# Performance work log

Measured on AMD Instinct MI355X. Metric: run time of the kernel, lower is better.

## Reference

```python
import jax, jax.numpy as jnp
import numpy as np

TEMPERATURE = 8.0  # sqrt(d_k=64)

def setup_inputs() -> dict:
    key = jax.random.key(0)
    kq, kk, kv = jax.random.split(key, 3)
    B, S, D = 32, 2048, 64
    q = jax.random.normal(kq, (B, S, D), dtype=jnp.float32)
    k = jax.random.normal(kk, (B, S, D), dtype=jnp.float32)
    v = jax.random.normal(kv, (B, S, D), dtype=jnp.float32)
    return {"q": q, "k": k, "v": v}

def reference(q, k, v):
    # scores: [B, S_q, S_k]
    attn = jnp.einsum('bqd,bkd->bqk', q, k) / TEMPERATURE
    attn = jax.nn.softmax(attn, axis=2)
    # dropout is identity in eval mode (deterministic reference baseline)
    output = jnp.einsum('bqk,bkd->bqd', attn, v)
    return (output, attn)
```

## Files before the change

kernel.cpp:

```cpp
#include <hip/hip_runtime.h>
#include <cstdint>
#include <cstddef>

#define B_    32
#define S_    2048
#define D_    64
#define QBLK  16
#define SLICE 264

typedef __attribute__((ext_vector_type(8))) short short8_t;
typedef __attribute__((ext_vector_type(4))) float f32x4;
typedef __attribute__((ext_vector_type(2))) unsigned u32x2;
typedef __attribute__((ext_vector_type(2))) float f32x2;

__device__ __forceinline__ short f2bf(float f) {
  union { float f; unsigned u; } x; x.f = f;
  unsigned u = x.u;
  u += 0x7fffu + ((u >> 16) & 1u);
  return (short)(u >> 16);
}
__device__ __forceinline__ float bf2f(unsigned s) {
  union { unsigned u; float f; } x;
  x.u = (s & 0xffffu) << 16;
  return x.f;
}

__global__ void convert_bf16_kernel(const float* __restrict__ in,
                                    short* __restrict__ out, int n4) {
  int i = blockIdx.x * blockDim.x + threadIdx.x;
  if (i >= n4) return;
  f32x4 f = ((const f32x4*)in)[i];
  short4 o;
  o.x = f2bf(f[0]); o.y = f2bf(f[1]); o.z = f2bf(f[2]); o.w = f2bf(f[3]);
  ((short4*)out)[i] = o;
}

__global__ void transpose_v_kernel(const float* __restrict__ v,
                                   short* __restrict__ vt) {
  __shared__ float t[64][65];
  int b   = blockIdx.x >> 5;
  int st  = blockIdx.x & 31;
  int tid = threadIdx.x;
  const float* src = v + ((size_t)(b * S_ + st * 64)) * D_;
#pragma unroll
  for (int p = 0; p < 4; ++p) {
    int r = p * 16 + (tid >> 4);
    int c = (tid & 15) * 4;
    f32x4 f = *(const f32x4*)(src + (size_t)r * D_ + c);
    t[r][c] = f[0]; t[r][c+1] = f[1]; t[r][c+2] = f[2]; t[r][c+3] = f[3];
  }
  __syncthreads();
#pragma unroll
  for (int p = 0; p < 8; ++p) {
    int d  = p * 8 + (tid >> 5);
    int si = (tid & 31) * 2;
    unsigned lo = (unsigned short)f2bf(t[si][d]);
    unsigned hi = (unsigned short)f2bf(t[si + 1][d]);
    *(unsigned*)(vt + ((size_t)(b * D_ + d)) * S_ + st * 64 + si) = lo | (hi << 16);
  }
}

template <bool WS>
__global__ __launch_bounds__(512, 4)
void attn_kernel(const float* __restrict__ q, const float* __restrict__ k,
                 const float* __restrict__ v, const short* __restrict__ Kb,
                 const short* __restrict__ Vt, float* __restrict__ out,
                 float* __restrict__ attn) {
  __shared__ short P_s[8][QBLK][SLICE];
  __shared__ float rs[QBLK];
  __shared__ float Obuf[QBLK][66];

  const int tid  = threadIdx.x;
  const int lane = tid & 63;
  const int wv   = tid >> 6;
  const int lr   = lane & 15;
  const int lq   = lane >> 4;

  const int nwg  = gridDim.x;
  const int per  = nwg >> 3;
  const int bid0 = blockIdx.x;
  const int bid  = (bid0 & 7) * per + (bid0 >> 3);

  const int b     = bid >> 7;
  const int qbase = (bid & 127) * QBLK;
  const int wcol  = wv * 256;

  if (tid < QBLK) rs[tid] = 0.f;
  for (int i = tid; i < QBLK * 66; i += 512) ((float*)Obuf)[i] = 0.f;
  __syncthreads();

  short8_t qf[2];
  {
    const float* qp = q + ((size_t)(b * S_ + qbase + lr)) * D_ + lq * 8;
#pragma unroll
    for (int kp = 0; kp < 2; ++kp) {
      f32x4 f0 = *(const f32x4*)(qp + kp * 32);
      f32x4 f1 = *(const f32x4*)(qp + kp * 32 + 4);
      short8_t a;
      a[0] = f2bf(f0[0]); a[1] = f2bf(f0[1]); a[2] = f2bf(f0[2]); a[3] = f2bf(f0[3]);
      a[4] = f2bf(f1[0]); a[5] = f2bf(f1[1]); a[6] = f2bf(f1[2]); a[7] = f2bf(f1[3]);
      qf[kp] = a;
    }
  }

  f32x4 acc[16];
#pragma unroll
  for (int ct = 0; ct < 16; ++ct) acc[ct] = (f32x4){0.f, 0.f, 0.f, 0.f};

#pragma unroll
  for (int ct = 0; ct < 16; ++ct) {
    int n = wcol + ct * 16 + lr;
    short8_t b0, b1;
    if constexpr (WS) {
      const short* kr = Kb + ((size_t)(b * S_ + n)) * D_ + lq * 8;
      b0 = *(const short8_t*)(kr);
      b1 = *(const short8_t*)(kr + 32);
    } else {
      const float* kr = k + ((size_t)(b * S_ + n)) * D_ + lq * 8;
      f32x4 f0 = *(const f32x4*)(kr);
      f32x4 f1 = *(const f32x4*)(kr + 4);
      f32x4 f2 = *(const f32x4*)(kr + 32);
      f32x4 f3 = *(const f32x4*)(kr + 36);
      b0[0]=f2bf(f0[0]); b0[1]=f2bf(f0[1]); b0[2]=f2bf(f0[2]); b0[3]=f2bf(f0[3]);
      b0[4]=f2bf(f1[0]); b0[5]=f2bf(f1[1]); b0[6]=f2bf(f1[2]); b0[7]=f2bf(f1[3]);
      b1[0]=f2bf(f2[0]); b1[1]=f2bf(f2[1]); b1[2]=f2bf(f2[2]); b1[3]=f2bf(f2[3]);
      b1[4]=f2bf(f3[0]); b1[5]=f2bf(f3[1]); b1[6]=f2bf(f3[2]); b1[7]=f2bf(f3[3]);
    }
    acc[ct] = __builtin_amdgcn_mfma_f32_16x16x32_bf16(b0, qf[0], acc[ct], 0, 0, 0);
    acc[ct] = __builtin_amdgcn_mfma_f32_16x16x32_bf16(b1, qf[1], acc[ct], 0, 0, 0);
  }

  float s0 = 0.f, s1 = 0.f, s2 = 0.f, s3 = 0.f;
#pragma unroll
  for (int ct = 0; ct < 16; ++ct) {
    float p0 = __expf(acc[ct][0] * 0.125f);
    float p1 = __expf(acc[ct][1] * 0.125f);
    float p2 = __expf(acc[ct][2] * 0.125f);
    float p3 = __expf(acc[ct][3] * 0.125f);
    s0 += p0; s1 += p1; s2 += p2; s3 += p3;
    u32x2 pk;
    pk[0] = (unsigned)(unsigned short)f2bf(p0) |
            ((unsigned)(unsigned short)f2bf(p1) << 16);
    pk[1] = (unsigned)(unsigned short)f2bf(p2) |
            ((unsigned)(unsigned short)f2bf(p3) << 16);
    *(u32x2*)&P_s[wv][lr][ct * 16 + lq * 4] = pk;
  }
  float s = (s0 + s1) + (s2 + s3);
  s += __shfl_xor(s, 16);
  s += __shfl_xor(s, 32);
  if (lane < 16) atomicAdd(&rs[lr], s);

  f32x4 oacc[4];
#pragma unroll
  for (int dt = 0; dt < 4; ++dt) oacc[dt] = (f32x4){0.f, 0.f, 0.f, 0.f};

#pragma unroll
  for (int ks = 0; ks < 8; ++ks) {
    short8_t pa = *(const short8_t*)&P_s[wv][lr][ks * 32 + lq * 8];
#pragma unroll
    for (int dt = 0; dt < 4; ++dt) {
      short8_t vb;
      if constexpr (WS) {
        vb = *(const short8_t*)(Vt + ((size_t)(b * D_ + dt * 16 + lr)) * S_
                                + wcol + ks * 32 + lq * 8);
      } else {
#pragma unroll
        for (int e = 0; e < 8; ++e)
          vb[e] = f2bf(v[((size_t)(b * S_ + wcol + ks * 32 + lq * 8 + e)) * D_
                         + dt * 16 + lr]);
      }
      oacc[dt] = __builtin_amdgcn_mfma_f32_16x16x32_bf16(pa, vb, oacc[dt], 0, 0, 0);
    }
  }
#pragma unroll
  for (int dt = 0; dt < 4; ++dt)
#pragma unroll
    for (int i = 0; i < 4; ++i)
      atomicAdd(&Obuf[lq * 4 + i][dt * 16 + lr], oacc[dt][i]);

  __syncthreads();

  {
    const int qq = tid >> 5;
    const int d0 = (tid & 31) * 2;
    const float rlq = 1.f / rs[qq];
    f32x2 o;
    o[0] = Obuf[qq][d0]     * rlq;
    o[1] = Obuf[qq][d0 + 1] * rlq;
    *(f32x2*)(out + ((size_t)(b * S_ + qbase + qq)) * D_ + d0) = o;
  }

#pragma unroll
  for (int r = 0; r < QBLK; ++r) {
    const float rlr = 1.f / rs[r];
    u32x2 pk = *(const u32x2*)&P_s[wv][r][lane * 4];
    f32x4 o;
    o[0] = bf2f(pk[0])       * rlr;
    o[1] = bf2f(pk[0] >> 16) * rlr;
    o[2] = bf2f(pk[1])       * rlr;
    o[3] = bf2f(pk[1] >> 16) * rlr;
    __builtin_nontemporal_store(
        o, (f32x4*)(attn + ((size_t)b * S_ + qbase + r) * S_ + wcol + lane * 4));
  }
}

extern "C" void kernel_launch(void* const* d_in, const int* in_sizes, int n_in,
                              void* d_out, int out_size, void* d_ws, size_t ws_size,
                              hipStream_t stream) {
  (void)in_sizes; (void)n_in; (void)out_size;
  const float* q = (const float*)d_in[0];
  const float* k = (const float*)d_in[1];
  const float* v = (const float*)d_in[2];
  float* out  = (float*)d_out;
  float* attn = out + (size_t)B_ * S_ * D_;

  const size_t nelem  = (size_t)B_ * S_ * D_;
  const size_t needKV = nelem * 2 * sizeof(short);

  dim3 grid(B_ * (S_ / QBLK));
  if (d_ws != nullptr && ws_size >= needKV) {
    short* Kb = (short*)d_ws;
    short* Vt = Kb + nelem;
    convert_bf16_kernel<<<(int)((nelem / 4 + 255) / 256), 256, 0, stream>>>(k, Kb, (int)(nelem / 4));
    transpose_v_kernel<<<B_ * (S_ / 64), 256, 0, stream>>>(v, Vt);
    attn_kernel<true><<<grid, 512, 0, stream>>>(q, k, v, Kb, Vt, out, attn);
  } else {
    attn_kernel<false><<<grid, 512, 0, stream>>>(q, k, v, nullptr, nullptr, out, attn);
  }
}
```

Before: 323.6 us.

## Split attention-matrix normalization into a separate bf16-to-fp32 expand kernel

When the workspace is large enough, the attention kernel writes unnormalized bf16 probabilities and per-row reciprocal sums to workspace, using sc1-flagged stores. A new grid-stride expand kernel then reads them back, scales them, and writes the fp32 attention matrix. This moves the large fp32 attention store out of the MFMA kernel, aiming to shorten its tail and raise throughput. The cost is an extra bf16 write and read of the full score matrix, plus one more kernel launch, and it needs a much larger workspace.

```diff
diff --git a/kernel.cpp b/kernel.cpp
--- a/kernel.cpp
+++ b/kernel.cpp
@@ -23,6 +23,11 @@
   union { unsigned u; float f; } x;
   x.u = (s & 0xffffu) << 16;
   return x.f;
+}
+
+__device__ __forceinline__ void store_sc1_b64(void* addr, u32x2 v) {
+  asm volatile("global_store_dwordx2 %0, %1, off sc1"
+               :: "v"(addr), "v"(v) : "memory");
 }
 
 __global__ void convert_bf16_kernel(const float* __restrict__ in,
@@ -60,12 +65,30 @@
   }
 }
 
-template <bool WS>
+__global__ __launch_bounds__(256)
+void expand_kernel(const unsigned* __restrict__ P, const float* __restrict__ rinv,
+                   float* __restrict__ attn, long n4) {
+  long i      = (long)blockIdx.x * blockDim.x + threadIdx.x;
+  long stride = (long)gridDim.x * blockDim.x;
+  for (; i < n4; i += stride) {
+    u32x2 pk = *((const u32x2*)P + i);
+    float rl = rinv[i >> 9];
+    f32x4 o;
+    o[0] = bf2f(pk[0])       * rl;
+    o[1] = bf2f(pk[0] >> 16) * rl;
+    o[2] = bf2f(pk[1])       * rl;
+    o[3] = bf2f(pk[1] >> 16) * rl;
+    *((f32x4*)attn + i) = o;
+  }
+}
+
+template <bool WS, bool SPLIT>
 __global__ __launch_bounds__(512, 4)
 void attn_kernel(const float* __restrict__ q, const float* __restrict__ k,
                  const float* __restrict__ v, const short* __restrict__ Kb,
                  const short* __restrict__ Vt, float* __restrict__ out,
-                 float* __restrict__ attn) {
+                 float* __restrict__ attn, short* __restrict__ Pws,
+                 float* __restrict__ rinv_ws) {
   __shared__ short P_s[8][QBLK][SLICE];
   __shared__ float rs[QBLK];
   __shared__ float Obuf[QBLK][66];
@@ -150,6 +173,14 @@
   s += __shfl_xor(s, 32);
   if (lane < 16) atomicAdd(&rs[lr], s);
 
+  if constexpr (SPLIT) {
+#pragma unroll
+    for (int r = 0; r < QBLK; ++r) {
+      u32x2 pk = *(const u32x2*)&P_s[wv][r][lane * 4];
+      store_sc1_b64(Pws + ((size_t)(b * S_ + qbase + r)) * S_ + wcol + lane * 4, pk);
+    }
+  }
+
   f32x4 oacc[4];
 #pragma unroll
   for (int dt = 0; dt < 4; ++dt) oacc[dt] = (f32x4){0.f, 0.f, 0.f, 0.f};
@@ -189,18 +220,23 @@
     o[1] = Obuf[qq][d0 + 1] * rlq;
     *(f32x2*)(out + ((size_t)(b * S_ + qbase + qq)) * D_ + d0) = o;
   }
-
-#pragma unroll
-  for (int r = 0; r < QBLK; ++r) {
-    const float rlr = 1.f / rs[r];
-    u32x2 pk = *(const u32x2*)&P_s[wv][r][lane * 4];
-    f32x4 o;
-    o[0] = bf2f(pk[0])       * rlr;
-    o[1] = bf2f(pk[0] >> 16) * rlr;
-    o[2] = bf2f(pk[1])       * rlr;
-    o[3] = bf2f(pk[1] >> 16) * rlr;
-    __builtin_nontemporal_store(
-        o, (f32x4*)(attn + ((size_t)b * S_ + qbase + r) * S_ + wcol + lane * 4));
+  if constexpr (SPLIT) {
+    if (tid < QBLK) rinv_ws[b * S_ + qbase + tid] = 1.f / rs[tid];
+  }
+
+  if constexpr (!SPLIT) {
+#pragma unroll
+    for (int r = 0; r < QBLK; ++r) {
+      const float rlr = 1.f / rs[r];
+      u32x2 pk = *(const u32x2*)&P_s[wv][r][lane * 4];
+      f32x4 o;
+      o[0] = bf2f(pk[0])       * rlr;
+      o[1] = bf2f(pk[0] >> 16) * rlr;
+      o[2] = bf2f(pk[1])       * rlr;
+      o[3] = bf2f(pk[1] >> 16) * rlr;
+      __builtin_nontemporal_store(
+          o, (f32x4*)(attn + ((size_t)b * S_ + qbase + r) * S_ + wcol + lane * 4));
+    }
   }
 }
 
@@ -216,15 +252,27 @@
 
   const size_t nelem  = (size_t)B_ * S_ * D_;
   const size_t needKV = nelem * 2 * sizeof(short);
+  const size_t nRows  = (size_t)B_ * S_;
+  const size_t nP     = (size_t)B_ * S_ * S_;
+  const size_t needAll = needKV + nRows * sizeof(float) + nP * sizeof(short);
 
   dim3 grid(B_ * (S_ / QBLK));
-  if (d_ws != nullptr && ws_size >= needKV) {
+  if (d_ws != nullptr && ws_size >= needAll) {
+    short* Kb   = (short*)d_ws;
+    short* Vt   = Kb + nelem;
+    float* rinv = (float*)(Vt + nelem);
+    short* Pws  = (short*)(rinv + nRows);
+    convert_bf16_kernel<<<(int)((nelem / 4 + 255) / 256), 256, 0, stream>>>(k, Kb, (int)(nelem / 4));
+    transpose_v_kernel<<<B_ * (S_ / 64), 256, 0, stream>>>(v, Vt);
+    attn_kernel<true, true><<<grid, 512, 0, stream>>>(q, k, v, Kb, Vt, out, attn, Pws, rinv);
+    expand_kernel<<<2048, 256, 0, stream>>>((const unsigned*)Pws, rinv, attn, (long)(nP / 4));
+  } else if (d_ws != nullptr && ws_size >= needKV) {
     short* Kb = (short*)d_ws;
     short* Vt = Kb + nelem;
     convert_bf16_kernel<<<(int)((nelem / 4 + 255) / 256), 256, 0, stream>>>(k, Kb, (int)(nelem / 4));
     transpose_v_kernel<<<B_ * (S_ / 64), 256, 0, stream>>>(v, Vt);
-    attn_kernel<true><<<grid, 512, 0, stream>>>(q, k, v, Kb, Vt, out, attn);
+    attn_kernel<true, false><<<grid, 512, 0, stream>>>(q, k, v, Kb, Vt, out, attn, nullptr, nullptr);
   } else {
-    attn_kernel<false><<<grid, 512, 0, stream>>>(q, k, v, nullptr, nullptr, out, attn);
-  }
-}
+    attn_kernel<false, false><<<grid, 512, 0, stream>>>(q, k, v, nullptr, nullptr, out, attn, nullptr, nullptr);
+  }
+}
```

Measured after the change: 486.0 us. +50.2%, slower.
